# Kernel optimization log

Measured on AMD Instinct MI355X. Metric: run time of the kernel, lower is better.

The kernel has to match this reference:

```python
import jax, jax.numpy as jnp
import numpy as np

B, T, C = 4, 2048, 1024
E = 8           # num_experts
H = 4 * C       # expert hidden dim


def setup_inputs() -> dict:
    key = jax.random.key(0)
    ks = jax.random.split(key, 4)
    s = 0.02
    return {
        "x":  jax.random.normal(ks[0], (B, T, C), jnp.float32),
        "Wr": jax.random.normal(ks[1], (C, E), jnp.float32) * s,
        "br": jnp.zeros((E,), jnp.float32),
        "W1": jax.random.normal(ks[2], (E, C, H), jnp.float32) * s,
        "b1": jnp.zeros((E, H), jnp.float32),
        "W2": jax.random.normal(ks[3], (E, H, C), jnp.float32) * s,
        "b2": jnp.zeros((E, C), jnp.float32),
    }


def reference(x, Wr, br, W1, b1, W2, b2):
    Bs, Ts, Cs = x.shape
    n_exp = W1.shape[0]
    xf = x.reshape(-1, Cs)                      # [N, C]
    logits = xf @ Wr + br                       # [N, E]
    gates = jax.nn.softmax(logits, axis=-1)
    probs = gates.max(axis=-1)                  # top-1 gate value [N]
    idx = gates.argmax(axis=-1)                 # expert assignment [N]

    # Masked-dense dispatch: each expert processes all tokens, mask zeroes
    # non-assigned tokens (same math as gather/MLP/scatter in the original;
    # a fused grouped-GEMM kernel would avoid the redundant FLOPs).
    out = jnp.zeros_like(xf)
    for e in range(n_exp):
        h = jax.nn.gelu(xf @ W1[e] + b1[e], approximate=False)  # [N, H]
        y = h @ W2[e] + b2[e]                                   # [N, C]
        g = jnp.where(idx == e, probs, 0.0)                     # [N]
        out = out + g[:, None] * y

    # load-balance aux loss (counts are non-differentiable, as in torch no_grad)
    counts = jnp.bincount(idx, length=n_exp).astype(jnp.float32)
    frac = counts / jnp.maximum(counts.sum(), 1.0)
    uniform = 1.0 / n_exp
    aux = jnp.mean((frac - uniform) ** 2)

    return out.reshape(Bs, Ts, Cs), aux
```

## Files before the change

### kernel.cpp

```cpp
#include <hip/hip_runtime.h>
#include <hip/hip_bf16.h>
#include <stdint.h>

#define N_TOK 8192
#define C_DIM 1024
#define E_NUM 8
#define H_DIM 4096
#define ROWS_PAD 9216
#define HBLK 32

typedef __attribute__((ext_vector_type(8))) short bf16x8;
typedef __attribute__((ext_vector_type(4))) float f32x4;

static __device__ __forceinline__ unsigned short f2bf(float f) {
    union { float f; unsigned u; } v; v.f = f;
    unsigned r = (v.u + 0x7FFFu + ((v.u >> 16) & 1u)) >> 16;
    return (unsigned short)r;
}

static __device__ __forceinline__ void load_lds16(const unsigned short* g, unsigned short* l) {
    __builtin_amdgcn_global_load_lds(
        (const __attribute__((address_space(1))) unsigned int*)g,
        (__attribute__((address_space(3))) unsigned int*)l, 16, 0, 0);
}

__global__ void transpose_w(const float* __restrict__ in, unsigned short* __restrict__ out,
                            int K, int N) {
    int e  = blockIdx.z;
    int n0 = blockIdx.x * 64;
    int k0 = blockIdx.y * 256;
    int t = threadIdx.x;
    int lane = t & 63;
    int w = t >> 6;
    const float* ip = in + (size_t)e * K * N;
    unsigned short* op = out + (size_t)e * N * K;
    int n = n0 + lane;
    for (int kb = k0 + w * 8; kb < k0 + 256; kb += 32) {
        float v[8];
#pragma unroll
        for (int j = 0; j < 8; j++) v[j] = ip[(size_t)(kb + j) * N + n];
        uint4 pk;
        pk.x = (unsigned)f2bf(v[0]) | ((unsigned)f2bf(v[1]) << 16);
        pk.y = (unsigned)f2bf(v[2]) | ((unsigned)f2bf(v[3]) << 16);
        pk.z = (unsigned)f2bf(v[4]) | ((unsigned)f2bf(v[5]) << 16);
        pk.w = (unsigned)f2bf(v[6]) | ((unsigned)f2bf(v[7]) << 16);
        *(uint4*)&op[(size_t)n * K + kb] = pk;
    }
}

__global__ void router_kernel(const float* __restrict__ x, const float* __restrict__ Wr,
                              const float* __restrict__ br,
                              float* __restrict__ probs, int* __restrict__ eidx) {
    int n = blockIdx.x * 4 + (threadIdx.x >> 6);
    int lane = threadIdx.x & 63;
    const float* xr = x + (size_t)n * C_DIM;
    double acc[E_NUM];
#pragma unroll
    for (int e = 0; e < E_NUM; e++) acc[e] = 0.0;
    for (int i = 0; i < 16; i++) {
        int c = i * 64 + lane;
        float xv = xr[c];
        const float4* wr = (const float4*)(Wr + c * E_NUM);
        float4 w0 = wr[0], w1 = wr[1];
        acc[0] += (double)xv * w0.x; acc[1] += (double)xv * w0.y;
        acc[2] += (double)xv * w0.z; acc[3] += (double)xv * w0.w;
        acc[4] += (double)xv * w1.x; acc[5] += (double)xv * w1.y;
        acc[6] += (double)xv * w1.z; acc[7] += (double)xv * w1.w;
    }
#pragma unroll
    for (int e = 0; e < E_NUM; e++) {
#pragma unroll
        for (int o = 32; o > 0; o >>= 1) acc[e] += __shfl_xor(acc[e], o, 64);
    }
    if (lane == 0) {
        float l[E_NUM];
        for (int e = 0; e < E_NUM; e++) l[e] = (float)acc[e] + br[e];
        int arg = 0; float m = l[0];
        for (int e = 1; e < E_NUM; e++) if (l[e] > m) { m = l[e]; arg = e; }
        float s = 0.f;
        for (int e = 0; e < E_NUM; e++) s += expf(l[e] - m);
        probs[n] = 1.0f / s;
        eidx[n] = arg;
    }
}

__global__ void hist_kernel(const int* __restrict__ eidx, int* __restrict__ blk_cnt) {
    __shared__ int lh[E_NUM];
    int t = threadIdx.x, b = blockIdx.x;
    if (t < E_NUM) lh[t] = 0;
    __syncthreads();
    atomicAdd(&lh[eidx[b * 256 + t]], 1);
    __syncthreads();
    if (t < E_NUM) blk_cnt[b * E_NUM + t] = lh[t];
}

__global__ void finalize_kernel(const int* __restrict__ blk_cnt, int* __restrict__ cnt,
                                int* __restrict__ seg, int* __restrict__ blockbase,
                                float* __restrict__ aux_out) {
    if (threadIdx.x == 0) {
        int tot[E_NUM];
        for (int e = 0; e < E_NUM; e++) tot[e] = 0;
        for (int b = 0; b < HBLK; b++)
            for (int e = 0; e < E_NUM; e++) tot[e] += blk_cnt[b * E_NUM + e];
        int off = 0;
        for (int e = 0; e < E_NUM; e++) {
            cnt[e] = tot[e];
            seg[e] = off;
            off += ((tot[e] + 127) >> 7) << 7;
        }
        int run[E_NUM];
        for (int e = 0; e < E_NUM; e++) run[e] = seg[e];
        for (int b = 0; b < HBLK; b++)
            for (int e = 0; e < E_NUM; e++) {
                blockbase[b * E_NUM + e] = run[e];
                run[e] += blk_cnt[b * E_NUM + e];
            }
        float s = 0.f;
        for (int e = 0; e < E_NUM; e++) {
            float fr = (float)tot[e] / (float)N_TOK - 1.0f / E_NUM;
            s += fr * fr;
        }
        aux_out[0] = s / (float)E_NUM;
    }
}

__global__ void gatherpos_kernel(const float* __restrict__ probs, const int* __restrict__ eidx,
                                 const int* __restrict__ blockbase, int* __restrict__ tok_row,
                                 int* __restrict__ inv_row, float* __restrict__ rowprob) {
    __shared__ int lh[E_NUM];
    int t = threadIdx.x, b = blockIdx.x;
    if (t < E_NUM) lh[t] = 0;
    __syncthreads();
    int n = b * 256 + t;
    int e = eidx[n];
    int lrank = atomicAdd(&lh[e], 1);
    int row = blockbase[b * E_NUM + e] + lrank;
    tok_row[n] = row;
    inv_row[row] = n;
    rowprob[row] = probs[n];
}

__global__ void copy_kernel(const float* __restrict__ x, const int* __restrict__ tok_row,
                            unsigned short* __restrict__ xg) {
    int n = blockIdx.x * 4 + (threadIdx.x >> 6);
    int lane = threadIdx.x & 63;
    int row = tok_row[n];
    const float2* xr = (const float2*)(x + (size_t)n * C_DIM);
    unsigned* xgr = (unsigned*)(xg + (size_t)row * C_DIM);
#pragma unroll
    for (int i = 0; i < 8; i++) {
        float2 v = xr[i * 64 + lane];
        xgr[i * 64 + lane] = (unsigned)f2bf(v.x) | ((unsigned)f2bf(v.y) << 16);
    }
}

template <int KDIM, int NDIM, int EPI>
__global__ __launch_bounds__(256) void moe_gemm(
    const unsigned short* __restrict__ Ag, const unsigned short* __restrict__ Bt,
    const float* __restrict__ bias, unsigned short* __restrict__ hg,
    float* __restrict__ out, const int* __restrict__ cnt, const int* __restrict__ seg,
    const int* __restrict__ inv_row, const float* __restrict__ rowprob) {
    int mt = blockIdx.y;
    int e;
    for (e = 0; e < E_NUM; e++) {
        int te = (cnt[e] + 127) >> 7;
        if (mt < te) break;
        mt -= te;
    }
    if (e >= E_NUM) return;
    int row0 = seg[e] + mt * 128;
    int col0 = blockIdx.x * 128;

    __shared__ unsigned short As[128 * 32];
    __shared__ unsigned short Bs[128 * 32];

    const unsigned short* Ab = Ag + (size_t)row0 * KDIM;
    const unsigned short* Bb = Bt + (size_t)e * NDIM * KDIM + (size_t)col0 * KDIM;

    int tid = threadIdx.x;
    int lane = tid & 63;
    int wv = tid >> 6;
    int wr = (wv >> 1) * 64, wc = (wv & 1) * 64;

    f32x4 acc[4][4] = {};

    int srow = lane >> 2;
    int scol = (lane & 3) * 8;

    for (int kk = 0; kk < KDIM; kk += 32) {
#pragma unroll
        for (int r = 0; r < 2; r++) {
            int chunk = wv + 4 * r;
            int rowa = 16 * chunk + srow;
            load_lds16(Ab + (size_t)rowa * KDIM + kk + scol, &As[16 * chunk * 32]);
            load_lds16(Bb + (size_t)rowa * KDIM + kk + scol, &Bs[16 * chunk * 32]);
        }
        __syncthreads();
        bf16x8 af[4], bfr[4];
        int fr = lane & 15, fq = (lane >> 4) * 8;
#pragma unroll
        for (int i = 0; i < 4; i++) {
            af[i]  = *(const bf16x8*)&As[(wr + i * 16 + fr) * 32 + fq];
            bfr[i] = *(const bf16x8*)&Bs[(wc + i * 16 + fr) * 32 + fq];
        }
#pragma unroll
        for (int i = 0; i < 4; i++)
#pragma unroll
            for (int j = 0; j < 4; j++)
                acc[i][j] = __builtin_amdgcn_mfma_f32_16x16x32_bf16(af[i], bfr[j], acc[i][j], 0, 0, 0);
        __syncthreads();
    }

    int cl = lane & 15, rq = (lane >> 4) * 4;
#pragma unroll
    for (int i = 0; i < 4; i++) {
#pragma unroll
        for (int j = 0; j < 4; j++) {
            int gcol = col0 + wc + j * 16 + cl;
            float b = bias[e * NDIM + gcol];
#pragma unroll
            for (int r = 0; r < 4; r++) {
                int grow = row0 + wr + i * 16 + rq + r;
                float v = acc[i][j][r] + b;
                if (EPI == 1) {
                    v = 0.5f * v * (1.0f + erff(v * 0.70710678118654752f));
                    hg[(size_t)grow * NDIM + gcol] = f2bf(v);
                } else {
                    int token = inv_row[grow];
                    if (token >= 0) out[(size_t)token * NDIM + gcol] = rowprob[grow] * v;
                }
            }
        }
    }
}

extern "C" void kernel_launch(void* const* d_in, const int* in_sizes, int n_in,
                              void* d_out, int out_size, void* d_ws, size_t ws_size,
                              hipStream_t stream) {
    const float* x  = (const float*)d_in[0];
    const float* Wr = (const float*)d_in[1];
    const float* br = (const float*)d_in[2];
    const float* W1 = (const float*)d_in[3];
    const float* b1 = (const float*)d_in[4];
    const float* W2 = (const float*)d_in[5];
    const float* b2 = (const float*)d_in[6];
    float* out = (float*)d_out;

    char* ws = (char*)d_ws;
    unsigned short* W1t = (unsigned short*)ws;
    unsigned short* W2t = (unsigned short*)(ws + (64ull << 20));
    unsigned short* xg  = (unsigned short*)(ws + (128ull << 20));
    unsigned short* hg  = (unsigned short*)(ws + (128ull << 20) + 18874368ull);
    char* small = ws + (128ull << 20) + 18874368ull + 75497472ull;
    float* probs     = (float*)small;
    int*   eidx      = (int*)(small + 32768);
    float* rowprob   = (float*)(small + 65536);
    int*   inv_row   = (int*)(small + 65536 + 36864);
    int*   tok_row   = (int*)(small + 65536 + 73728);
    int*   blk_cnt   = (int*)(small + 65536 + 73728 + 32768);
    int*   blockbase = blk_cnt + HBLK * E_NUM;
    int*   cnt       = blockbase + HBLK * E_NUM;
    int*   seg       = cnt + 8;

    hipMemsetAsync(xg, 0, (size_t)ROWS_PAD * C_DIM * 2, stream);
    hipMemsetAsync(inv_row, 0xFF, ROWS_PAD * 4, stream);

    transpose_w<<<dim3(H_DIM / 64, C_DIM / 256, E_NUM), 256, 0, stream>>>(W1, W1t, C_DIM, H_DIM);
    transpose_w<<<dim3(C_DIM / 64, H_DIM / 256, E_NUM), 256, 0, stream>>>(W2, W2t, H_DIM, C_DIM);

    router_kernel<<<N_TOK / 4, 256, 0, stream>>>(x, Wr, br, probs, eidx);
    hist_kernel<<<HBLK, 256, 0, stream>>>(eidx, blk_cnt);
    finalize_kernel<<<1, 64, 0, stream>>>(blk_cnt, cnt, seg, blockbase,
                                          out + (size_t)N_TOK * C_DIM);
    gatherpos_kernel<<<HBLK, 256, 0, stream>>>(probs, eidx, blockbase, tok_row, inv_row, rowprob);
    copy_kernel<<<N_TOK / 4, 256, 0, stream>>>(x, tok_row, xg);

    moe_gemm<C_DIM, H_DIM, 1><<<dim3(H_DIM / 128, 72), 256, 0, stream>>>(
        xg, W1t, b1, hg, nullptr, cnt, seg, inv_row, rowprob);
    moe_gemm<H_DIM, C_DIM, 2><<<dim3(C_DIM / 128, 72), 256, 0, stream>>>(
        hg, W2t, b2, nullptr, out, cnt, seg, inv_row, rowprob);
}
```

Measured before the change: 743.8 us.

## Swizzle LDS with K=64 tiles, split-K second GEMM, LDS-tiled weight transpose

The weight transpose now stages a 64x64 tile in padded shared memory so both global reads and writes are coalesced. The grouped GEMM loads K=64 per step into an XOR-swizzled LDS layout to reduce bank conflicts and halve barrier count. The down-projection is split over K into two chunks and accumulated with float atomics into a zeroed output, which adds parallelism at the cost of an extra memset and atomic traffic.

```diff
diff --git a/kernel.cpp b/kernel.cpp
--- a/kernel.cpp
+++ b/kernel.cpp
@@ -26,25 +26,26 @@
 
 __global__ void transpose_w(const float* __restrict__ in, unsigned short* __restrict__ out,
                             int K, int N) {
-    int e  = blockIdx.z;
-    int n0 = blockIdx.x * 64;
-    int k0 = blockIdx.y * 256;
-    int t = threadIdx.x;
-    int lane = t & 63;
-    int w = t >> 6;
-    const float* ip = in + (size_t)e * K * N;
-    unsigned short* op = out + (size_t)e * N * K;
-    int n = n0 + lane;
-    for (int kb = k0 + w * 8; kb < k0 + 256; kb += 32) {
-        float v[8];
-#pragma unroll
-        for (int j = 0; j < 8; j++) v[j] = ip[(size_t)(kb + j) * N + n];
-        uint4 pk;
-        pk.x = (unsigned)f2bf(v[0]) | ((unsigned)f2bf(v[1]) << 16);
-        pk.y = (unsigned)f2bf(v[2]) | ((unsigned)f2bf(v[3]) << 16);
-        pk.z = (unsigned)f2bf(v[4]) | ((unsigned)f2bf(v[5]) << 16);
-        pk.w = (unsigned)f2bf(v[6]) | ((unsigned)f2bf(v[7]) << 16);
-        *(uint4*)&op[(size_t)n * K + kb] = pk;
+    __shared__ unsigned short lt[64 * 65];
+    int e = blockIdx.z;
+    int n0 = blockIdx.x * 64, k0 = blockIdx.y * 64;
+    int t = threadIdx.x, lane = t & 63, w = t >> 6;
+    const float* ip = in + (size_t)e * K * N + (size_t)k0 * N + n0;
+    unsigned short* op = out + (size_t)e * N * K + (size_t)n0 * K + k0;
+#pragma unroll
+    for (int r = 0; r < 16; r++) {
+        int k = w * 16 + r;
+        lt[lane * 65 + k] = f2bf(ip[(size_t)k * N + lane]);
+    }
+    __syncthreads();
+#pragma unroll
+    for (int p = 0; p < 2; p++) {
+        int idx = p * 256 + t;
+        int n = idx >> 3, kc = (idx & 7) * 8;
+        union { uint4 v; unsigned short u[8]; } pk;
+#pragma unroll
+        for (int j = 0; j < 8; j++) pk.u[j] = lt[n * 65 + kc + j];
+        *(uint4*)&op[(size_t)n * K + kc] = pk.v;
     }
 }
 
@@ -154,7 +155,7 @@
     }
 }
 
-template <int KDIM, int NDIM, int EPI>
+template <int KCHUNK, int KDIM, int NDIM, int EPI>
 __global__ __launch_bounds__(256) void moe_gemm(
     const unsigned short* __restrict__ Ag, const unsigned short* __restrict__ Bt,
     const float* __restrict__ bias, unsigned short* __restrict__ hg,
@@ -170,9 +171,10 @@
     if (e >= E_NUM) return;
     int row0 = seg[e] + mt * 128;
     int col0 = blockIdx.x * 128;
-
-    __shared__ unsigned short As[128 * 32];
-    __shared__ unsigned short Bs[128 * 32];
+    int kk0 = blockIdx.z * KCHUNK;
+
+    __shared__ unsigned short As[128 * 64];
+    __shared__ unsigned short Bs[128 * 64];
 
     const unsigned short* Ab = Ag + (size_t)row0 * KDIM;
     const unsigned short* Bb = Bt + (size_t)e * NDIM * KDIM + (size_t)col0 * KDIM;
@@ -184,40 +186,50 @@
 
     f32x4 acc[4][4] = {};
 
-    int srow = lane >> 2;
-    int scol = (lane & 3) * 8;
-
-    for (int kk = 0; kk < KDIM; kk += 32) {
-#pragma unroll
-        for (int r = 0; r < 2; r++) {
-            int chunk = wv + 4 * r;
-            int rowa = 16 * chunk + srow;
-            load_lds16(Ab + (size_t)rowa * KDIM + kk + scol, &As[16 * chunk * 32]);
-            load_lds16(Bb + (size_t)rowa * KDIM + kk + scol, &Bs[16 * chunk * 32]);
+    int lsub = lane >> 3;
+    int cg8 = ((lane & 7) ^ lsub) * 8;
+
+    int fr = lane & 15;
+    int fq = lane >> 4;
+
+    for (int kk = kk0; kk < kk0 + KCHUNK; kk += 64) {
+#pragma unroll
+        for (int m = 0; m < 4; m++) {
+            int blk = wv * 4 + m;
+            int rowa = blk * 8 + lsub;
+            load_lds16(Ab + (size_t)rowa * KDIM + kk + cg8, &As[blk * 512]);
+            load_lds16(Bb + (size_t)rowa * KDIM + kk + cg8, &Bs[blk * 512]);
         }
         __syncthreads();
-        bf16x8 af[4], bfr[4];
-        int fr = lane & 15, fq = (lane >> 4) * 8;
-#pragma unroll
-        for (int i = 0; i < 4; i++) {
-            af[i]  = *(const bf16x8*)&As[(wr + i * 16 + fr) * 32 + fq];
-            bfr[i] = *(const bf16x8*)&Bs[(wc + i * 16 + fr) * 32 + fq];
-        }
-#pragma unroll
-        for (int i = 0; i < 4; i++)
-#pragma unroll
-            for (int j = 0; j < 4; j++)
-                acc[i][j] = __builtin_amdgcn_mfma_f32_16x16x32_bf16(af[i], bfr[j], acc[i][j], 0, 0, 0);
+#pragma unroll
+        for (int s = 0; s < 2; s++) {
+            bf16x8 af[4], bfr[4];
+#pragma unroll
+            for (int i = 0; i < 4; i++) {
+                int ra = wr + i * 16 + fr;
+                int ca = (fq + s * 4) ^ (ra & 7);
+                af[i] = *(const bf16x8*)&As[ra * 64 + ca * 8];
+                int rb = wc + i * 16 + fr;
+                int cb = (fq + s * 4) ^ (rb & 7);
+                bfr[i] = *(const bf16x8*)&Bs[rb * 64 + cb * 8];
+            }
+#pragma unroll
+            for (int i = 0; i < 4; i++)
+#pragma unroll
+                for (int j = 0; j < 4; j++)
+                    acc[i][j] = __builtin_amdgcn_mfma_f32_16x16x32_bf16(af[i], bfr[j], acc[i][j], 0, 0, 0);
+        }
         __syncthreads();
     }
 
     int cl = lane & 15, rq = (lane >> 4) * 4;
+    bool addb = (EPI == 1) || (blockIdx.z == 0);
 #pragma unroll
     for (int i = 0; i < 4; i++) {
 #pragma unroll
         for (int j = 0; j < 4; j++) {
             int gcol = col0 + wc + j * 16 + cl;
-            float b = bias[e * NDIM + gcol];
+            float b = addb ? bias[e * NDIM + gcol] : 0.0f;
 #pragma unroll
             for (int r = 0; r < 4; r++) {
                 int grow = row0 + wr + i * 16 + rq + r;
@@ -227,7 +239,8 @@
                     hg[(size_t)grow * NDIM + gcol] = f2bf(v);
                 } else {
                     int token = inv_row[grow];
-                    if (token >= 0) out[(size_t)token * NDIM + gcol] = rowprob[grow] * v;
+                    if (token >= 0)
+                        unsafeAtomicAdd(&out[(size_t)token * NDIM + gcol], rowprob[grow] * v);
                 }
             }
         }
@@ -264,9 +277,10 @@
 
     hipMemsetAsync(xg, 0, (size_t)ROWS_PAD * C_DIM * 2, stream);
     hipMemsetAsync(inv_row, 0xFF, ROWS_PAD * 4, stream);
-
-    transpose_w<<<dim3(H_DIM / 64, C_DIM / 256, E_NUM), 256, 0, stream>>>(W1, W1t, C_DIM, H_DIM);
-    transpose_w<<<dim3(C_DIM / 64, H_DIM / 256, E_NUM), 256, 0, stream>>>(W2, W2t, H_DIM, C_DIM);
+    hipMemsetAsync(out, 0, (size_t)out_size * 4, stream);
+
+    transpose_w<<<dim3(H_DIM / 64, C_DIM / 64, E_NUM), 256, 0, stream>>>(W1, W1t, C_DIM, H_DIM);
+    transpose_w<<<dim3(C_DIM / 64, H_DIM / 64, E_NUM), 256, 0, stream>>>(W2, W2t, H_DIM, C_DIM);
 
     router_kernel<<<N_TOK / 4, 256, 0, stream>>>(x, Wr, br, probs, eidx);
     hist_kernel<<<HBLK, 256, 0, stream>>>(eidx, blk_cnt);
@@ -275,8 +289,8 @@
     gatherpos_kernel<<<HBLK, 256, 0, stream>>>(probs, eidx, blockbase, tok_row, inv_row, rowprob);
     copy_kernel<<<N_TOK / 4, 256, 0, stream>>>(x, tok_row, xg);
 
-    moe_gemm<C_DIM, H_DIM, 1><<<dim3(H_DIM / 128, 72), 256, 0, stream>>>(
+    moe_gemm<C_DIM, C_DIM, H_DIM, 1><<<dim3(H_DIM / 128, 72, 1), 256, 0, stream>>>(
         xg, W1t, b1, hg, nullptr, cnt, seg, inv_row, rowprob);
-    moe_gemm<H_DIM, C_DIM, 2><<<dim3(C_DIM / 128, 72), 256, 0, stream>>>(
+    moe_gemm<H_DIM / 2, H_DIM, C_DIM, 2><<<dim3(C_DIM / 128, 72, 2), 256, 0, stream>>>(
         hg, W2t, b2, nullptr, out, cnt, seg, inv_row, rowprob);
 }
```

Measured after the change: 764.1 us. 1.03x slower.
